# Kernel optimization log

Hardware: AMD Instinct MI355X
Metric: run time of the kernel (lower is better)

## Reference

```python
import jax, jax.numpy as jnp
import numpy as np

NUM_TOKENS = 2048
HIDDEN = 2048
MOE_INTER = 1408
N_EXPERTS = 16
TOP_K = 4
N_SHARED = 2
SHARED_INTER = N_SHARED * MOE_INTER  # 2816
CAPACITY = 768
ROUTED_SCALE = 1.0


def setup_inputs() -> dict:
    key = jax.random.key(0)
    ks = jax.random.split(key, 9)
    s = 0.02  # init scale for stability
    return {
        "hidden_states": jax.random.normal(ks[0], (NUM_TOKENS, HIDDEN), jnp.float32),
        "w_gate": jax.random.normal(ks[1], (N_EXPERTS, HIDDEN), jnp.float32) * s,
        "w1": jax.random.normal(ks[2], (N_EXPERTS, HIDDEN, MOE_INTER), jnp.float32) * s,  # gate_proj
        "w3": jax.random.normal(ks[3], (N_EXPERTS, HIDDEN, MOE_INTER), jnp.float32) * s,  # up_proj
        "w2": jax.random.normal(ks[4], (N_EXPERTS, MOE_INTER, HIDDEN), jnp.float32) * s,  # down_proj
        "ws1": jax.random.normal(ks[5], (HIDDEN, SHARED_INTER), jnp.float32) * s,
        "ws3": jax.random.normal(ks[6], (HIDDEN, SHARED_INTER), jnp.float32) * s,
        "ws2": jax.random.normal(ks[7], (SHARED_INTER, HIDDEN), jnp.float32) * s,
    }


def _moe_forward(x, w_gate, w1, w3, w2, ws1, ws3, ws2):
    T, d = x.shape
    E = w1.shape[0]
    # ---- router: softmax scores, top-k selection (DeepSeek-V2, norm_topk_prob=False) ----
    scores = jax.nn.softmax(x @ w_gate.T, axis=-1)            # [T, E]
    topw, topi = jax.lax.top_k(scores, TOP_K)                 # [T, K]
    topw = topw * ROUTED_SCALE
    flat_e = topi.reshape(-1)                                 # [T*K] expert id per slot
    flat_w = topw.reshape(-1)                                 # [T*K]
    tok_ids = jnp.repeat(jnp.arange(T), TOP_K)                # [T*K]
    # ---- dispatch: position of each slot within its expert's buffer ----
    onehot = jax.nn.one_hot(flat_e, E, dtype=jnp.int32)       # [T*K, E]
    pos = jnp.take_along_axis(jnp.cumsum(onehot, axis=0), flat_e[:, None], axis=1)[:, 0] - 1
    valid = (pos < CAPACITY).astype(x.dtype)
    buf = jnp.zeros((E, CAPACITY, d), x.dtype).at[flat_e, pos].set(x[tok_ids], mode='drop')
    # ---- grouped SwiGLU expert FFN ----
    g = jnp.einsum('ecd,edi->eci', buf, w1)
    u = jnp.einsum('ecd,edi->eci', buf, w3)
    o = jnp.einsum('eci,eid->ecd', jax.nn.silu(g) * u, w2)    # [E, C, d]
    # ---- combine: gather back, weight, scatter-add per token ----
    gathered = o[flat_e, jnp.clip(pos, 0, CAPACITY - 1)] * (flat_w * valid)[:, None]
    routed = jax.ops.segment_sum(gathered, tok_ids, num_segments=T)  # [T, d]
    # ---- shared experts (always-on SwiGLU) ----
    shared = (jax.nn.silu(x @ ws1) * (x @ ws3)) @ ws2
    return routed + shared


def reference(hidden_states, w_gate, w1, w3, w2, ws1, ws3, ws2):
    return _moe_forward(hidden_states, w_gate, w1, w3, w2, ws1, ws3, ws2)
```

## Files before the change

### kernel.cpp

```cpp
#include <hip/hip_runtime.h>
#include <hip/hip_bf16.h>
#include <cstdint>

#define T_TOKENS 2048
#define HIDDEN 2048
#define INTER 1408
#define NEXP 16
#define TOPK 4
#define SINTER 2816
#define CAP 768
#define BK 32

typedef __attribute__((ext_vector_type(8))) short short8;
typedef __attribute__((ext_vector_type(8))) unsigned short ushort8;
typedef __attribute__((ext_vector_type(4))) float f32x4;

__device__ __forceinline__ float4 ld4f(const float* p) {
  return *reinterpret_cast<const float4*>(p);
}

__device__ __forceinline__ unsigned short f2bf(float v) {
  unsigned int u = __float_as_uint(v);
  unsigned int r = (u + 0x7FFFu + ((u >> 16) & 1u)) >> 16;
  return (unsigned short)r;
}

__device__ __forceinline__ void gld16(const void* g, void* l) {
  __builtin_amdgcn_global_load_lds(
      (const __attribute__((address_space(1))) void*)g,
      (__attribute__((address_space(3))) void*)l, 16, 0, 0);
}

__global__ __launch_bounds__(64) void router_kernel(
    const float* __restrict__ x, const float* __restrict__ wg,
    int* __restrict__ topi, float* __restrict__ topw)
{
  const int t = blockIdx.x;
  const int lane = threadIdx.x;
  float acc[NEXP];
#pragma unroll
  for (int e = 0; e < NEXP; ++e) acc[e] = 0.f;
  const float* xr = x + (size_t)t * HIDDEN;
  for (int i = lane; i < HIDDEN; i += 64) {
    float xv = xr[i];
#pragma unroll
    for (int e = 0; e < NEXP; ++e) acc[e] += xv * wg[e * HIDDEN + i];
  }
#pragma unroll
  for (int e = 0; e < NEXP; ++e) {
#pragma unroll
    for (int off = 32; off > 0; off >>= 1)
      acc[e] += __shfl_xor(acc[e], off);
  }
  float m = acc[0];
#pragma unroll
  for (int e = 1; e < NEXP; ++e) m = fmaxf(m, acc[e]);
  float p[NEXP];
  float s = 0.f;
#pragma unroll
  for (int e = 0; e < NEXP; ++e) { p[e] = expf(acc[e] - m); s += p[e]; }
  const float inv = 1.f / s;
#pragma unroll
  for (int e = 0; e < NEXP; ++e) p[e] *= inv;
  if (lane == 0) {
#pragma unroll
    for (int k = 0; k < TOPK; ++k) {
      float best = -1.f; int bi = 0;
#pragma unroll
      for (int e = 0; e < NEXP; ++e)
        if (p[e] > best) { best = p[e]; bi = e; }
      topi[t * TOPK + k] = bi;
      topw[t * TOPK + k] = best;
      p[bi] = -1.f;
    }
  }
}

__global__ __launch_bounds__(1024) void partition_kernel(
    const int* __restrict__ topi, float* __restrict__ topw,
    int* __restrict__ rowtok, int* __restrict__ count)
{
  __shared__ int se[T_TOKENS * TOPK];
  for (int i = threadIdx.x; i < T_TOKENS * TOPK; i += 1024) se[i] = topi[i];
  __syncthreads();

  const int wave = threadIdx.x >> 6;
  const int lane = threadIdx.x & 63;
  const uint64_t below = (lane == 0) ? 0ull : ((~0ull) >> (64 - lane));
  int base = 0;
  for (int c = 0; c < T_TOKENS * TOPK; c += 64) {
    int ev = se[c + lane];
    uint64_t mask = __ballot(ev == wave);
    if (ev == wave) {
      int my = base + __popcll(mask & below);
      if (my < CAP) rowtok[wave * CAP + my] = c + lane;
      else          topw[c + lane] = 0.f;
    }
    base += __popcll(mask);
  }
  if (lane == 0) count[wave] = base < CAP ? base : CAP;
}

__global__ __launch_bounds__(256) void cvt_x_kernel(
    const float* __restrict__ x, unsigned short* __restrict__ xb)
{
  const long i = ((long)blockIdx.x * 256 + threadIdx.x) * 8;
  float4 a = ld4f(x + i), b = ld4f(x + i + 4);
  float v[8] = {a.x, a.y, a.z, a.w, b.x, b.y, b.z, b.w};
  unsigned short o[8];
#pragma unroll
  for (int j = 0; j < 8; ++j) o[j] = f2bf(v[j]);
  *(ushort8*)(xb + i) = *(ushort8*)&o[0];
}

__global__ __launch_bounds__(256) void tcvt_w_kernel(
    const float* __restrict__ W0, const float* __restrict__ W1,
    unsigned short* __restrict__ T,
    int K, int N, long tz, int mul, int nz0, int which0, int which1)
{
  const int z = blockIdx.z;
  const float* W; int which; long zz;
  if (z < nz0) { W = W0; which = which0; zz = z; }
  else         { W = W1; which = which1; zz = z - nz0; }
  W += zz * (long)K * N;
  T += zz * tz;
  const int k0 = blockIdx.x * 64, n0 = blockIdx.y * 64;
  __shared__ float tile[64][65];
  const int tr = threadIdx.x >> 4;
  const int tc4 = (threadIdx.x & 15) * 4;
#pragma unroll
  for (int p = 0; p < 4; ++p) {
    int r = p * 16 + tr;
    float4 v = ld4f(W + (long)(k0 + r) * N + n0 + tc4);
    tile[r][tc4] = v.x; tile[r][tc4 + 1] = v.y;
    tile[r][tc4 + 2] = v.z; tile[r][tc4 + 3] = v.w;
  }
  __syncthreads();
  const int wn = threadIdx.x >> 3;
  const int wk = (threadIdx.x & 7) * 8;
#pragma unroll
  for (int p = 0; p < 2; ++p) {
    int n = p * 32 + wn;
    unsigned short o[8];
#pragma unroll
    for (int j = 0; j < 8; ++j) o[j] = f2bf(tile[wk + j][n]);
    const int gn = n0 + n;
    const long prow = ((long)(gn >> 4) * mul + which) * 16 + (gn & 15);
    *(ushort8*)(T + prow * K + k0 + wk) = *(ushort8*)&o[0];
  }
}

template<int NW, int EPI>
__global__ __launch_bounds__(NW * 64, 2)
void gemm_bf(const unsigned short* __restrict__ Ag, int ldka,
             const unsigned short* __restrict__ Bg, long bstride,
             float* __restrict__ C, unsigned short* __restrict__ H, int ldc,
             const float* __restrict__ TW,
             const int* __restrict__ arows_g, int ashift, long aexp,
             const int* __restrict__ crows_g, long cexp,
             const int* __restrict__ cnt, int Mfix, int K,
             int MT, int NTn)
{
  constexpr int TN = NW * 32;
  constexpr int GA = 8 / NW;
  constexpr int WN = NW / 2;

  const int nwg = gridDim.x;
  const int lin = (blockIdx.x & 7) * (nwg >> 3) + (blockIdx.x >> 3);
  const int mt = lin % MT;
  const int rest = lin / MT;
  const int nt = rest % NTn;
  const int e = rest / NTn;

  const int M = cnt ? cnt[e] : Mfix;
  if (mt * 128 >= M) return;
  const int n0 = nt * TN;

  const int tid = threadIdx.x;
  const int l = tid & 63;
  const int w = tid >> 6;
  const int wm = w / WN;
  const int wn = w % WN;
  const int fr = l & 15;
  const int fc = l >> 4;

  const int* arows = arows_g ? arows_g + e * CAP : nullptr;
  const int* crows = crows_g ? crows_g + e * CAP : nullptr;
  const unsigned short* Bexp = Bg + (long)e * bstride;

  __shared__ __align__(16) unsigned short sA[3][128 * BK];
  __shared__ __align__(16) unsigned short sB[3][TN * BK];

  const int rb_s = ((l >> 3) & 1) | (((l >> 5) & 1) << 1);
  const int sch = ((l & 3) ^ rb_s) * 8;
  long aoff[GA], boff[2];
#pragma unroll
  for (int j = 0; j < GA; ++j) {
    const int rloc = (w * GA + j) * 16 + (l >> 2);
    int r = mt * 128 + rloc;
    if (r > M - 1) r = M - 1;
    const long arow = arows ? (long)(arows[r] >> ashift) : (aexp * e + r);
    aoff[j] = arow * (long)ldka + sch;
  }
#pragma unroll
  for (int j = 0; j < 2; ++j) {
    const int rloc = (w * 2 + j) * 16 + (l >> 2);
    boff[j] = (long)(n0 + rloc) * K + sch;
  }

  const int rb_r = ((fr >> 1) & 1) | (((fr >> 3) & 1) << 1);
  const int pcoff = (fc ^ rb_r) * 8;

  f32x4 acc[4][4];
#pragma unroll
  for (int i = 0; i < 4; ++i)
#pragma unroll
    for (int j = 0; j < 4; ++j) acc[i][j] = (f32x4)0.f;

  const int NT = K / BK;

  auto stage = [&](int buf, int kt) {
#pragma unroll
    for (int j = 0; j < GA; ++j)
      gld16(Ag + aoff[j] + kt, &sA[buf][(w * GA + j) * 16 * BK]);
#pragma unroll
    for (int j = 0; j < 2; ++j)
      gld16(Bexp + boff[j] + kt, &sB[buf][(w * 2 + j) * 16 * BK]);
  };

  stage(0, 0);
  stage(1, BK);

  int rb = 0, wb = 2;
  for (int t = 0; t < NT; ++t) {
    if (t + 1 < NT) {
      if constexpr (NW == 8) asm volatile("s_waitcnt vmcnt(3)" ::: "memory");
      else                   asm volatile("s_waitcnt vmcnt(4)" ::: "memory");
    } else {
      asm volatile("s_waitcnt vmcnt(0)" ::: "memory");
    }
    __builtin_amdgcn_s_barrier();
    __builtin_amdgcn_sched_barrier(0);

    if (t + 2 < NT) stage(wb, (t + 2) * BK);

    short8 fa[4], fb[4];
#pragma unroll
    for (int mi = 0; mi < 4; ++mi)
      fa[mi] = *(const short8*)&sA[rb][(wm * 64 + mi * 16 + fr) * BK + pcoff];
#pragma unroll
    for (int ni = 0; ni < 4; ++ni)
      fb[ni] = *(const short8*)&sB[rb][(wn * 64 + ni * 16 + fr) * BK + pcoff];
#pragma unroll
    for (int mi = 0; mi < 4; ++mi)
#pragma unroll
      for (int ni = 0; ni < 4; ++ni)
        acc[mi][ni] = __builtin_amdgcn_mfma_f32_16x16x32_bf16(fa[mi], fb[ni], acc[mi][ni], 0, 0, 0);

    rb = (rb == 2) ? 0 : rb + 1;
    wb = (wb == 2) ? 0 : wb + 1;
  }

#pragma unroll
  for (int mi = 0; mi < 4; ++mi)
#pragma unroll
    for (int rr = 0; rr < 4; ++rr) {
      const int r = mt * 128 + wm * 64 + mi * 16 + fc * 4 + rr;
      if (r >= M) continue;
      if constexpr (EPI == 2) {
        const long crow = crows ? (long)crows[r] : (cexp * e + r);
#pragma unroll
        for (int np = 0; np < 2; ++np) {
          const float g = acc[mi][2 * np][rr];
          const float u = acc[mi][2 * np + 1][rr];
          const float h = u * (g / (1.f + __expf(-g)));
          const int i = (n0 / 32 + wn * 2 + np) * 16 + fr;
          H[crow * (long)ldc + i] = f2bf(h);
        }
      } else if constexpr (EPI == 3) {
        const int slot = crows[r];
        const float wgt = TW[slot];
        if (wgt != 0.f) {
          const long tok = slot >> 2;
#pragma unroll
          for (int ni = 0; ni < 4; ++ni) {
            const int col = n0 + wn * 64 + ni * 16 + fr;
            atomicAdd(&C[tok * (long)ldc + col], wgt * acc[mi][ni][rr]);
          }
        }
      } else {
        const long crow = crows ? (long)crows[r] : (cexp * e + r);
#pragma unroll
        for (int ni = 0; ni < 4; ++ni) {
          const int col = n0 + wn * 64 + ni * 16 + fr;
          C[crow * (long)ldc + col] = acc[mi][ni][rr];
        }
      }
    }
}

extern "C" void kernel_launch(void* const* d_in, const int* in_sizes, int n_in,
                              void* d_out, int out_size, void* d_ws, size_t ws_size,
                              hipStream_t stream)
{
  const float* x   = (const float*)d_in[0];
  const float* wg  = (const float*)d_in[1];
  const float* w1  = (const float*)d_in[2];
  const float* w3  = (const float*)d_in[3];
  const float* w2  = (const float*)d_in[4];
  const float* ws1 = (const float*)d_in[5];
  const float* ws3 = (const float*)d_in[6];
  const float* ws2 = (const float*)d_in[7];
  float* out = (float*)d_out;

  char* w = (char*)d_ws;
  int*   topi   = (int*)w;   w += (size_t)T_TOKENS * TOPK * 4;
  float* topw   = (float*)w; w += (size_t)T_TOKENS * TOPK * 4;
  int*   rowtok = (int*)w;   w += (size_t)NEXP * CAP * 4;
  int*   count  = (int*)w;   w += 256;
  uintptr_t a = (uintptr_t)w; a = (a + 255) & ~(uintptr_t)255; w = (char*)a;

  const size_t XSZ  = (size_t)T_TOKENS * HIDDEN;
  const size_t WSI  = (size_t)2 * HIDDEN * SINTER;
  const size_t WRI  = (size_t)2 * NEXP * HIDDEN * INTER;
  const size_t HSSZ = (size_t)T_TOKENS * SINTER;
  const size_t HRSZ = (size_t)NEXP * CAP * INTER;

  unsigned short* xb  = (unsigned short*)w; w += XSZ * 2;
  unsigned short* wSi = (unsigned short*)w; w += WSI * 2;
  unsigned short* wRi = (unsigned short*)w; w += WRI * 2;
  unsigned short* hs  = (unsigned short*)w; w += HSSZ * 2;
  unsigned short* hr  = (unsigned short*)w; w += HRSZ * 2;
  unsigned short* wS2 = wSi;
  unsigned short* wR2 = wRi;

  router_kernel<<<T_TOKENS, 64, 0, stream>>>(x, wg, topi, topw);
  partition_kernel<<<1, 1024, 0, stream>>>(topi, topw, rowtok, count);
  cvt_x_kernel<<<(int)(XSZ / (256 * 8)), 256, 0, stream>>>(x, xb);

  tcvt_w_kernel<<<dim3(HIDDEN / 64, SINTER / 64, 2), 256, 0, stream>>>(
      ws1, ws3, wSi, HIDDEN, SINTER, 0L, 2, 1, 0, 1);
  gemm_bf<4, 2><<<(T_TOKENS / 128) * (2 * SINTER / 128), 256, 0, stream>>>(
      xb, HIDDEN, wSi, 0L, nullptr, hs, SINTER, nullptr,
      nullptr, 0, 0L, nullptr, 0L,
      nullptr, T_TOKENS, HIDDEN, T_TOKENS / 128, 2 * SINTER / 128);

  tcvt_w_kernel<<<dim3(HIDDEN / 64, INTER / 64, 2 * NEXP), 256, 0, stream>>>(
      w1, w3, wRi, HIDDEN, INTER, (long)2 * HIDDEN * INTER, 2, NEXP, 0, 1);
  gemm_bf<4, 2><<<(CAP / 128) * (2 * INTER / 128) * NEXP, 256, 0, stream>>>(
      xb, HIDDEN, wRi, (long)2 * HIDDEN * INTER, nullptr, hr, INTER, nullptr,
      rowtok, 2, 0L, nullptr, (long)CAP,
      count, 0, HIDDEN, CAP / 128, 2 * INTER / 128);

  tcvt_w_kernel<<<dim3(SINTER / 64, HIDDEN / 64, 1), 256, 0, stream>>>(
      ws2, ws2, wS2, SINTER, HIDDEN, 0L, 1, 1, 0, 0);
  gemm_bf<4, 0><<<(T_TOKENS / 128) * (HIDDEN / 128), 256, 0, stream>>>(
      hs, SINTER, wS2, 0L, out, nullptr, HIDDEN, nullptr,
      nullptr, 0, 0L, nullptr, 0L,
      nullptr, T_TOKENS, SINTER, T_TOKENS / 128, HIDDEN / 128);

  tcvt_w_kernel<<<dim3(INTER / 64, HIDDEN / 64, NEXP), 256, 0, stream>>>(
      w2, w2, wR2, INTER, HIDDEN, (long)INTER * HIDDEN, 1, NEXP, 0, 0);
  gemm_bf<4, 3><<<(CAP / 128) * (HIDDEN / 128) * NEXP, 256, 0, stream>>>(
      hr, INTER, wR2, (long)INTER * HIDDEN, out, nullptr, HIDDEN, topw,
      nullptr, 0, (long)CAP, rowtok, 0L,
      count, 0, INTER, CAP / 128, HIDDEN / 128);
}
```

Baseline: 629.1 us.

## Fuse next-stage weight conversion blocks into each preceding GEMM launch

Moves the fp32-to-bf16 transpose and conversion of each upcoming weight set out of its standalone kernel. Each conversion now runs as extra trailing blocks appended to the grid of the previous GEMM launch, reusing that GEMM's shared-memory buffer as the transpose tile. The aim is to overlap the memory-bound weight conversion with compute-bound GEMM work and to remove several kernel launches. It depends on buffer aliasing staying safe, since wS2/wR2 reuse the wSi/wRi storage, and conversion blocks may compete with GEMM blocks for CU slots and bandwidth.

```diff
diff --git a/kernel.cpp b/kernel.cpp
--- a/kernel.cpp
+++ b/kernel.cpp
@@ -113,19 +113,18 @@
   *(ushort8*)(xb + i) = *(ushort8*)&o[0];
 }
 
-__global__ __launch_bounds__(256) void tcvt_w_kernel(
-    const float* __restrict__ W0, const float* __restrict__ W1,
-    unsigned short* __restrict__ T,
-    int K, int N, long tz, int mul, int nz0, int which0, int which1)
-{
-  const int z = blockIdx.z;
+__device__ __forceinline__ void tcvt_body(
+    int bx, int by, int bz,
+    const float* W0, const float* W1, unsigned short* T,
+    int K, int N, long tz, int mul, int nz0, int which0, int which1,
+    float (*tile)[65])
+{
   const float* W; int which; long zz;
-  if (z < nz0) { W = W0; which = which0; zz = z; }
-  else         { W = W1; which = which1; zz = z - nz0; }
+  if (bz < nz0) { W = W0; which = which0; zz = bz; }
+  else          { W = W1; which = which1; zz = bz - nz0; }
   W += zz * (long)K * N;
   T += zz * tz;
-  const int k0 = blockIdx.x * 64, n0 = blockIdx.y * 64;
-  __shared__ float tile[64][65];
+  const int k0 = bx * 64, n0 = by * 64;
   const int tr = threadIdx.x >> 4;
   const int tc4 = (threadIdx.x & 15) * 4;
 #pragma unroll
@@ -148,6 +147,16 @@
     const long prow = ((long)(gn >> 4) * mul + which) * 16 + (gn & 15);
     *(ushort8*)(T + prow * K + k0 + wk) = *(ushort8*)&o[0];
   }
+}
+
+__global__ __launch_bounds__(256) void tcvt_w_kernel(
+    const float* __restrict__ W0, const float* __restrict__ W1,
+    unsigned short* __restrict__ T,
+    int K, int N, long tz, int mul, int nz0, int which0, int which1)
+{
+  __shared__ float tile[64][65];
+  tcvt_body(blockIdx.x, blockIdx.y, blockIdx.z, W0, W1, T, K, N, tz, mul,
+            nz0, which0, which1, tile);
 }
 
 template<int NW, int EPI>
@@ -159,14 +168,30 @@
              const int* __restrict__ arows_g, int ashift, long aexp,
              const int* __restrict__ crows_g, long cexp,
              const int* __restrict__ cnt, int Mfix, int K,
-             int MT, int NTn)
+             int MT, int NTn,
+             const float* tW0, const float* tW1, unsigned short* tT,
+             int tK, int tN, long ttz, int tmul, int tnz0, int tw0, int tw1,
+             int tKX, int tNY, int gemmBlocks)
 {
   constexpr int TN = NW * 32;
   constexpr int GA = 8 / NW;
   constexpr int WN = NW / 2;
 
-  const int nwg = gridDim.x;
-  const int lin = (blockIdx.x & 7) * (nwg >> 3) + (blockIdx.x >> 3);
+  __shared__ __align__(16) unsigned short sA[3][128 * BK];
+  __shared__ __align__(16) unsigned short sB[3][TN * BK];
+
+  if ((int)blockIdx.x >= gemmBlocks) {
+    const int tbid = (int)blockIdx.x - gemmBlocks;
+    const int bx = tbid % tKX;
+    const int rest2 = tbid / tKX;
+    const int by = rest2 % tNY;
+    const int bz = rest2 / tNY;
+    tcvt_body(bx, by, bz, tW0, tW1, tT, tK, tN, ttz, tmul, tnz0, tw0, tw1,
+              (float(*)[65])&sA[0][0]);
+    return;
+  }
+
+  const int lin = (blockIdx.x & 7) * (gemmBlocks >> 3) + (blockIdx.x >> 3);
   const int mt = lin % MT;
   const int rest = lin / MT;
   const int nt = rest % NTn;
@@ -187,9 +212,6 @@
   const int* arows = arows_g ? arows_g + e * CAP : nullptr;
   const int* crows = crows_g ? crows_g + e * CAP : nullptr;
   const unsigned short* Bexp = Bg + (long)e * bstride;
-
-  __shared__ __align__(16) unsigned short sA[3][128 * BK];
-  __shared__ __align__(16) unsigned short sB[3][TN * BK];
 
   const int rb_s = ((l >> 3) & 1) | (((l >> 5) & 1) << 1);
   const int sch = ((l & 3) ^ rb_s) * 8;
@@ -340,29 +362,47 @@
 
   tcvt_w_kernel<<<dim3(HIDDEN / 64, SINTER / 64, 2), 256, 0, stream>>>(
       ws1, ws3, wSi, HIDDEN, SINTER, 0L, 2, 1, 0, 1);
-  gemm_bf<4, 2><<<(T_TOKENS / 128) * (2 * SINTER / 128), 256, 0, stream>>>(
-      xb, HIDDEN, wSi, 0L, nullptr, hs, SINTER, nullptr,
-      nullptr, 0, 0L, nullptr, 0L,
-      nullptr, T_TOKENS, HIDDEN, T_TOKENS / 128, 2 * SINTER / 128);
-
-  tcvt_w_kernel<<<dim3(HIDDEN / 64, INTER / 64, 2 * NEXP), 256, 0, stream>>>(
-      w1, w3, wRi, HIDDEN, INTER, (long)2 * HIDDEN * INTER, 2, NEXP, 0, 1);
-  gemm_bf<4, 2><<<(CAP / 128) * (2 * INTER / 128) * NEXP, 256, 0, stream>>>(
-      xb, HIDDEN, wRi, (long)2 * HIDDEN * INTER, nullptr, hr, INTER, nullptr,
-      rowtok, 2, 0L, nullptr, (long)CAP,
-      count, 0, HIDDEN, CAP / 128, 2 * INTER / 128);
-
-  tcvt_w_kernel<<<dim3(SINTER / 64, HIDDEN / 64, 1), 256, 0, stream>>>(
-      ws2, ws2, wS2, SINTER, HIDDEN, 0L, 1, 1, 0, 0);
-  gemm_bf<4, 0><<<(T_TOKENS / 128) * (HIDDEN / 128), 256, 0, stream>>>(
-      hs, SINTER, wS2, 0L, out, nullptr, HIDDEN, nullptr,
-      nullptr, 0, 0L, nullptr, 0L,
-      nullptr, T_TOKENS, SINTER, T_TOKENS / 128, HIDDEN / 128);
-
-  tcvt_w_kernel<<<dim3(INTER / 64, HIDDEN / 64, NEXP), 256, 0, stream>>>(
-      w2, w2, wR2, INTER, HIDDEN, (long)INTER * HIDDEN, 1, NEXP, 0, 0);
-  gemm_bf<4, 3><<<(CAP / 128) * (HIDDEN / 128) * NEXP, 256, 0, stream>>>(
-      hr, INTER, wR2, (long)INTER * HIDDEN, out, nullptr, HIDDEN, topw,
-      nullptr, 0, (long)CAP, rowtok, 0L,
-      count, 0, INTER, CAP / 128, HIDDEN / 128);
-}
+
+  {
+    const int G = (T_TOKENS / 128) * (2 * SINTER / 128);
+    const int TCVT = (HIDDEN / 64) * (INTER / 64) * (2 * NEXP);
+    gemm_bf<4, 2><<<G + TCVT, 256, 0, stream>>>(
+        xb, HIDDEN, wSi, 0L, nullptr, hs, SINTER, nullptr,
+        nullptr, 0, 0L, nullptr, 0L,
+        nullptr, T_TOKENS, HIDDEN, T_TOKENS / 128, 2 * SINTER / 128,
+        w1, w3, wRi, HIDDEN, INTER, (long)2 * HIDDEN * INTER, 2, NEXP, 0, 1,
+        HIDDEN / 64, INTER / 64, G);
+  }
+
+  {
+    const int G = (CAP / 128) * (2 * INTER / 128) * NEXP;
+    const int TCVT = (SINTER / 64) * (HIDDEN / 64);
+    gemm_bf<4, 2><<<G + TCVT, 256, 0, stream>>>(
+        xb, HIDDEN, wRi, (long)2 * HIDDEN * INTER, nullptr, hr, INTER, nullptr,
+        rowtok, 2, 0L, nullptr, (long)CAP,
+        count, 0, HIDDEN, CAP / 128, 2 * INTER / 128,
+        ws2, ws2, wS2, SINTER, HIDDEN, 0L, 1, 1, 0, 0,
+        SINTER / 64, HIDDEN / 64, G);
+  }
+
+  {
+    const int G = (T_TOKENS / 128) * (HIDDEN / 128);
+    const int TCVT = (INTER / 64) * (HIDDEN / 64) * NEXP;
+    gemm_bf<4, 0><<<G + TCVT, 256, 0, stream>>>(
+        hs, SINTER, wS2, 0L, out, nullptr, HIDDEN, nullptr,
+        nullptr, 0, 0L, nullptr, 0L,
+        nullptr, T_TOKENS, SINTER, T_TOKENS / 128, HIDDEN / 128,
+        w2, w2, wR2, INTER, HIDDEN, (long)INTER * HIDDEN, 1, NEXP, 0, 0,
+        INTER / 64, HIDDEN / 64, G);
+  }
+
+  {
+    const int G = (CAP / 128) * (HIDDEN / 128) * NEXP;
+    gemm_bf<4, 3><<<G, 256, 0, stream>>>(
+        hr, INTER, wR2, (long)INTER * HIDDEN, out, nullptr, HIDDEN, topw,
+        nullptr, 0, (long)CAP, rowtok, 0L,
+        count, 0, INTER, CAP / 128, HIDDEN / 128,
+        nullptr, nullptr, nullptr, 1, 1, 0L, 1, 1, 0, 0,
+        1, 1, G);
+  }
+}
```

Result: faster. 583.8 us (-7.2%).
